# Kernel optimization log

Hardware: AMD Instinct MI355X
Metric: run time of the kernel (lower is better)

The kernel has to match this reference:

```python
import jax, jax.numpy as jnp
import numpy as np

WINDOW = 3
RATIO = 5


def _box_filter(x, win):
    """Depthwise 3D box (mean) filter, 'same' padding, per channel.
    x: [N, C, D, H, W] -> [N, C, D, H, W]
    Matches torch conv3d with ones([1,1,w,w,w])/w^3 applied per channel.
    """
    c = x.shape[1]
    k = jnp.ones((c, 1, win, win, win), x.dtype) / (win ** 3)
    pad = win // 2
    return jax.lax.conv_general_dilated(
        x, k,
        window_strides=(1, 1, 1),
        padding=[(pad, pad)] * 3,
        dimension_numbers=('NCDHW', 'OIDHW', 'NCDHW'),
        feature_group_count=c,
    )


def setup_inputs() -> dict:
    key = jax.random.key(0)
    k1, k2 = jax.random.split(key)
    y_pred = jax.random.normal(k1, (1, 3, 192, 192, 192), dtype=jnp.float32)
    y_true = jax.random.uniform(k2, (1, 1, 192, 192, 192), dtype=jnp.float32)
    return {"y_pred": y_pred, "y_true": y_true}


def reference(y_pred, y_true):
    # Finite differences (abs), each [1, 3, D-1, H-1, W-1]
    base = y_pred[:, :, :-1, :-1, :-1]
    dy = jnp.abs(y_pred[:, :, 1:, :-1, :-1] - base)
    dx = jnp.abs(y_pred[:, :, :-1, 1:, :-1] - base)
    dz = jnp.abs(y_pred[:, :, :-1, :-1, 1:] - base)

    # 9 box-filtered single-channel maps == 3 depthwise box filters
    fx = _box_filter(dx, WINDOW)
    fy = _box_filter(dy, WINDOW)
    fz = _box_filter(dz, WINDOW)
    dxdx, dxdy, dxdz = fx[:, 1:2], fy[:, 1:2], fz[:, 1:2]
    dydx, dydy, dydz = fx[:, 0:1], fy[:, 0:1], fz[:, 0:1]
    dzdx, dzdy, dzdz = fx[:, 2:3], fy[:, 2:3], fz[:, 2:3]

    # Neo-Hookean invariants
    det_1 = (dxdx + 1) * ((dydy + 1) * (dzdz + 1) - dydz * dzdy)
    det_2 = -dxdy * (dydx * (dzdz + 1) - dydz * dzdx)
    det_3 = dxdz * (dydx * dzdy - (dydy + 1) * dzdx)
    J = det_1 + det_2 + det_3

    Tr = ((dxdx + 1) ** 2 + dxdy ** 2 + dxdz ** 2
          + dydx ** 2 + (dydy + 1) ** 2 + dydz ** 2
          + dzdx ** 2 + dzdy ** 2 + (dzdz + 1) ** 2)

    # mode == 'exp'
    stretch = Tr * jnp.exp(-J + 1) - 3
    vol_change = (J - 1) ** 2

    # Faithful replication of the sequential mu/lambda normalization in torch:
    mu = 1.0
    lam = mu * RATIO
    mu = mu / (mu + lam)          # 1/6
    lam = lam / (mu + lam)        # 30/31 (uses updated mu, as in source)

    U = mu / 2 * stretch + lam / 2 * vol_change
    return jnp.mean(U)
```

## Files before the change

### kernel.cpp

```cpp
#include <hip/hip_runtime.h>
#include <math.h>

#define DIM 192
#define OD  191
#define VOLX 7077888
#define TW 32
#define TH 16
#define NBW 6
#define NBH 12
#define CD  10
#define NCH 20

typedef _Float16 h4 __attribute__((ext_vector_type(4)));
typedef _Float16 h8 __attribute__((ext_vector_type(8)));
typedef unsigned int u2v __attribute__((ext_vector_type(2)));

static __device__ __forceinline__ h4 habs4(h4 v) {
    u2v u = __builtin_bit_cast(u2v, v);
    u &= 0x7FFF7FFFu;
    return __builtin_bit_cast(h4, u);
}

__global__ __launch_bounds__(256, 4)
void nh_fused_kernel(const float* __restrict__ P, float* __restrict__ out) {
    const int tid = threadIdx.x;
    const int tx  = tid & 15;
    const int ty  = tid >> 4;
    const int w0  = blockIdx.x * TW;
    const int h0  = blockIdx.y * TH;
    const int ds  = blockIdx.z * CD;
    const int de  = min(ds + CD, OD);

    __shared__ h4 sraw[2][19][36];
    __shared__ h8 sHD[18][35];
    __shared__ h4 sW[18][38];
    __shared__ float wsum[4];

    const int oh  = h0 + ty;
    const int ow0 = w0 + 2 * tx;
    const bool v0 = (oh < OD) && (ow0 < OD);
    const bool v1 = (oh < OD) && (ow0 + 1 < OD);
    const bool interior = (w0 >= 1) && (w0 + 33 <= OD) && (h0 >= 1) && (h0 + 17 <= OD);

    h8 rA0[2], rA1[2], rA2[2];
    h4 rW0[2], rW1[2], rW2[2];
    #pragma unroll
    for (int o = 0; o < 2; ++o) {
        rA0[o] = (h8)0; rA1[o] = (h8)0; rA2[o] = (h8)0;
        rW0[o] = (h4)0; rW1[o] = (h4)0; rW2[o] = (h4)0;
    }

    float acc = 0.f;

    for (int t = ds - 1; t <= de + 1; ++t) {
        const int cb = t & 1, pb = cb ^ 1;
        __syncthreads();

        if (t >= 0 && t < DIM) {
            const size_t pl = (size_t)t * (DIM * DIM);
            if (interior) {
                #pragma unroll
                for (int it = 0; it < 3; ++it) {
                    const int l = tid + it * 256;
                    if (l < 19 * 35) {
                        const int hh = l / 35, ww = l - hh * 35;
                        const size_t base = pl + (size_t)(h0 - 1 + hh) * DIM + (size_t)(w0 - 1 + ww);
                        const float x = P[base], y = P[base + VOLX], z = P[base + 2 * VOLX];
                        sraw[cb][hh][ww] = (h4){(_Float16)x, (_Float16)y, (_Float16)z, (_Float16)0.f};
                    }
                }
            } else {
                #pragma unroll
                for (int it = 0; it < 3; ++it) {
                    const int l = tid + it * 256;
                    if (l < 19 * 35) {
                        const int hh = l / 35, ww = l - hh * 35;
                        const int hp = h0 - 1 + hh, wp = w0 - 1 + ww;
                        float x = 0.f, y = 0.f, z = 0.f;
                        if (hp >= 0 && hp < DIM && wp >= 0 && wp < DIM) {
                            const size_t base = pl + (size_t)hp * DIM + (size_t)wp;
                            x = P[base]; y = P[base + VOLX]; z = P[base + 2 * VOLX];
                        }
                        sraw[cb][hh][ww] = (h4){(_Float16)x, (_Float16)y, (_Float16)z, (_Float16)0.f};
                    }
                }
            }
        }
        __syncthreads();

        const int p = t - 1;
        const bool pp = (t >= ds) && (p >= 0) && (p < OD);
        if (pp) {
            #pragma unroll
            for (int it = 0; it < 3; ++it) {
                const int l = tid + it * 256;
                if (l < 18 * 34) {
                    const int hh = l / 34, ww = l - hh * 34;
                    const h4 c = sraw[pb][hh][ww];
                    h4 hd = habs4(sraw[pb][hh + 1][ww] - c);
                    h4 wd = habs4(sraw[pb][hh][ww + 1] - c);
                    h4 dd = habs4(sraw[cb][hh][ww] - c);
                    if (!interior) {
                        const int hp = h0 - 1 + hh, wp = w0 - 1 + ww;
                        if (hp < 0 || hp >= OD || wp < 0 || wp >= OD) {
                            hd = (h4)0; dd = (h4)0; wd = (h4)0;
                        }
                    }
                    sHD[hh][ww] = __builtin_shufflevector(hd, dd, 0, 1, 2, 3, 4, 5, 6, 7);
                    sW[hh][ww]  = wd;
                }
            }
        }
        __syncthreads();

        #pragma unroll
        for (int o = 0; o < 2; ++o) {
            rA0[o] = rA1[o]; rA1[o] = rA2[o];
            rW0[o] = rW1[o]; rW1[o] = rW2[o];
        }
        if (pp) {
            h8 s0 = (h8)0, s1 = (h8)0;
            h4 q0 = (h4)0, q1 = (h4)0;
            #pragma unroll
            for (int j = 0; j < 3; ++j) {
                const h8 t0 = sHD[ty + j][2 * tx + 0];
                const h8 t1 = sHD[ty + j][2 * tx + 1];
                const h8 t2 = sHD[ty + j][2 * tx + 2];
                const h8 t3 = sHD[ty + j][2 * tx + 3];
                const h8 m = t1 + t2;
                s0 += t0 + m;
                s1 += t3 + m;
                const h8* rw = (const h8*)&sW[ty + j][2 * tx];
                const h8 u01 = rw[0];
                const h8 u23 = rw[1];
                const h4 u0 = __builtin_shufflevector(u01, u01, 0, 1, 2, 3);
                const h4 u1 = __builtin_shufflevector(u01, u01, 4, 5, 6, 7);
                const h4 u2 = __builtin_shufflevector(u23, u23, 0, 1, 2, 3);
                const h4 u3 = __builtin_shufflevector(u23, u23, 4, 5, 6, 7);
                const h4 mw = u1 + u2;
                q0 += u0 + mw;
                q1 += u3 + mw;
            }
            rA2[0] = s0; rA2[1] = s1; rW2[0] = q0; rW2[1] = q1;
        } else {
            rA2[0] = (h8)0; rA2[1] = (h8)0; rW2[0] = (h4)0; rW2[1] = (h4)0;
        }

        const int d = t - 2;
        if (d >= ds && d < de) {
            #pragma unroll
            for (int o = 0; o < 2; ++o) {
                if (o == 0 ? v0 : v1) {
                    const h8 FA = rA0[o] + rA1[o] + rA2[o];
                    const h4 FW = rW0[o] + rW1[o] + rW2[o];
                    const float inv27 = 1.f / 27.f;
                    const float dydx = (float)FA[0] * inv27, dxdx = (float)FA[1] * inv27, dzdx = (float)FA[2] * inv27;
                    const float dydy = (float)FA[4] * inv27, dxdy = (float)FA[5] * inv27, dzdy = (float)FA[6] * inv27;
                    const float dydz = (float)FW[0] * inv27, dxdz = (float)FW[1] * inv27, dzdz = (float)FW[2] * inv27;
                    const float a = dxdx + 1.f, e = dydy + 1.f, iN = dzdz + 1.f;
                    const float J = a * (e * iN - dydz * dzdy)
                                  - dxdy * (dydx * iN - dydz * dzdx)
                                  + dxdz * (dydx * dzdy - e * dzdx);
                    const float Tr = a * a + dxdy * dxdy + dxdz * dxdz
                                   + dydx * dydx + e * e + dydz * dydz
                                   + dzdx * dzdx + dzdy * dzdy + iN * iN;
                    const float stretch = Tr * __expf(1.f - J) - 3.f;
                    const float vol = (J - 1.f) * (J - 1.f);
                    acc += 0.0833333358f * stretch + 0.4838709677f * vol;
                }
            }
        }
    }

    acc *= (1.f / 6967871.f);

    #pragma unroll
    for (int off = 32; off > 0; off >>= 1) acc += __shfl_down(acc, off, 64);
    if ((tid & 63) == 0) wsum[tid >> 6] = acc;
    __syncthreads();
    if (tid == 0) {
        atomicAdd(out, wsum[0] + wsum[1] + wsum[2] + wsum[3]);
    }
}

extern "C" void kernel_launch(void* const* d_in, const int* in_sizes, int n_in,
                              void* d_out, int out_size, void* d_ws, size_t ws_size,
                              hipStream_t stream) {
    const float* y_pred = (const float*)d_in[0];
    float* out = (float*)d_out;

    hipMemsetAsync(out, 0, sizeof(float), stream);

    dim3 grid(NBW, NBH, NCH);
    nh_fused_kernel<<<grid, 256, 0, stream>>>(y_pred, out);
}
```

Baseline: 197.6 us.

## Prefetch next plane into registers and repack difference layout into fewer LDS slots

Restructures the depth loop so each plane's global loads are issued two iterations ahead into registers and written to LDS one iteration later. This overlaps memory latency with compute and removes one barrier per plane. It precomputes clamped offsets and masks once per thread, and packs two of the three W-difference channels into the spare slots of the h8 array, leaving only one half in a small side array, which cuts LDS traffic. The depth chunk shrinks to 8 and the occupancy hint rises to 6 blocks per CU. In exchange it adds register pressure and more halo recompute from the shorter depth chunks.

Result: faster. 192.7 us (-2.5%).

```diff
diff --git a/kernel.cpp b/kernel.cpp
--- a/kernel.cpp
+++ b/kernel.cpp
@@ -3,16 +3,26 @@
 
 #define DIM 192
 #define OD  191
+#define PLN 36864
 #define VOLX 7077888
 #define TW 32
 #define TH 16
 #define NBW 6
 #define NBH 12
-#define CD  10
-#define NCH 20
-
-typedef _Float16 h4 __attribute__((ext_vector_type(4)));
-typedef _Float16 h8 __attribute__((ext_vector_type(8)));
+#define CD  8
+#define NCH 24
+
+#define RH 19
+#define RW 35
+#define NS (RH*RW)
+#define DH 18
+#define DW 34
+#define ND (DH*DW)
+#define SBW 34
+
+typedef _Float16 h2v __attribute__((ext_vector_type(2)));
+typedef _Float16 h4  __attribute__((ext_vector_type(4)));
+typedef _Float16 h8  __attribute__((ext_vector_type(8)));
 typedef unsigned int u2v __attribute__((ext_vector_type(2)));
 
 static __device__ __forceinline__ h4 habs4(h4 v) {
@@ -21,93 +31,116 @@
     return __builtin_bit_cast(h4, u);
 }
 
-__global__ __launch_bounds__(256, 4)
+__global__ __launch_bounds__(256, 6)
 void nh_fused_kernel(const float* __restrict__ P, float* __restrict__ out) {
     const int tid = threadIdx.x;
-    const int tx  = tid & 15;
-    const int ty  = tid >> 4;
-    const int w0  = blockIdx.x * TW;
-    const int h0  = blockIdx.y * TH;
-    const int ds  = blockIdx.z * CD;
-    const int de  = min(ds + CD, OD);
-
-    __shared__ h4 sraw[2][19][36];
-    __shared__ h8 sHD[18][35];
-    __shared__ h4 sW[18][38];
+    const int tx = tid & 15, ty = tid >> 4;
+    const int w0 = blockIdx.x * TW, h0 = blockIdx.y * TH;
+    const int ds = blockIdx.z * CD;
+    const int de = min(ds + CD, OD);
+    const int lastP = min(de + 1, DIM - 1);
+
+    __shared__ h4  sraw[2][RH][RW];
+    __shared__ h8  sA[DH][RW];
+    __shared__ h2v sB[DH][SBW];
     __shared__ float wsum[4];
 
-    const int oh  = h0 + ty;
-    const int ow0 = w0 + 2 * tx;
+    const int oh = h0 + ty, ow0 = w0 + 2 * tx;
     const bool v0 = (oh < OD) && (ow0 < OD);
     const bool v1 = (oh < OD) && (ow0 + 1 < OD);
-    const bool interior = (w0 >= 1) && (w0 + 33 <= OD) && (h0 >= 1) && (h0 + 17 <= OD);
+
+    int  sLin[3], sOff[3];
+    bool sMask[3], sAct[3];
+    #pragma unroll
+    for (int i = 0; i < 3; ++i) {
+        int l = tid + 256 * i;
+        sAct[i] = (l < NS);
+        l = min(l, NS - 1);
+        const int sh = l / RW, sw = l - sh * RW;
+        const int hp = h0 - 1 + sh, wp = w0 - 1 + sw;
+        sMask[i] = (hp >= 0) && (hp < DIM) && (wp >= 0) && (wp < DIM);
+        sOff[i]  = min(max(hp, 0), DIM - 1) * DIM + min(max(wp, 0), DIM - 1);
+        sLin[i]  = l;
+    }
+
+    int  dLin[3], dLinB[3];
+    bool dAct[3], dOut[3];
+    #pragma unroll
+    for (int i = 0; i < 3; ++i) {
+        int l = tid + 256 * i;
+        dAct[i] = (l < ND);
+        l = min(l, ND - 1);
+        const int dh = l / DW, dw = l - dh * DW;
+        const int hp = h0 - 1 + dh, wp = w0 - 1 + dw;
+        dOut[i]  = (hp < 0) || (hp >= OD) || (wp < 0) || (wp >= OD);
+        dLin[i]  = dh * RW + dw;
+        dLinB[i] = dh * SBW + dw;
+    }
+
+    float px[3][3];
+    #pragma unroll
+    for (int i = 0; i < 3; ++i) { px[i][0] = px[i][1] = px[i][2] = 0.f; }
+
+    auto issue = [&](int q) {
+        #pragma unroll
+        for (int i = 0; i < 3; ++i) {
+            if (sAct[i]) {
+                const float* b = P + (size_t)q * PLN + sOff[i];
+                px[i][0] = b[0]; px[i][1] = b[VOLX]; px[i][2] = b[2 * VOLX];
+            }
+        }
+    };
+    auto store = [&](int slot) {
+        h4* dst = &sraw[slot][0][0];
+        #pragma unroll
+        for (int i = 0; i < 3; ++i) {
+            if (sAct[i]) {
+                h4 v = sMask[i] ? (h4){(_Float16)px[i][0], (_Float16)px[i][1],
+                                       (_Float16)px[i][2], (_Float16)0.f}
+                                : (h4)0;
+                dst[sLin[i]] = v;
+            }
+        }
+    };
+
+    if (ds >= 1) { issue(ds - 1); store((ds - 1) & 1); }
+    issue(ds);
 
     h8 rA0[2], rA1[2], rA2[2];
-    h4 rW0[2], rW1[2], rW2[2];
+    _Float16 rB0[2], rB1[2], rB2[2];
     #pragma unroll
     for (int o = 0; o < 2; ++o) {
         rA0[o] = (h8)0; rA1[o] = (h8)0; rA2[o] = (h8)0;
-        rW0[o] = (h4)0; rW1[o] = (h4)0; rW2[o] = (h4)0;
-    }
-
+        rB0[o] = (_Float16)0.f; rB1[o] = (_Float16)0.f; rB2[o] = (_Float16)0.f;
+    }
     float acc = 0.f;
 
-    for (int t = ds - 1; t <= de + 1; ++t) {
-        const int cb = t & 1, pb = cb ^ 1;
+    for (int p = ds - 1; p <= de; ++p) {
+        const int sp = p & 1, sn = sp ^ 1;
+        const bool pv = (p >= 0) && (p < OD);
+
+        if (p + 1 <= lastP) store(sn);
+        if (p + 2 <= lastP) issue(p + 2);
         __syncthreads();
 
-        if (t >= 0 && t < DIM) {
-            const size_t pl = (size_t)t * (DIM * DIM);
-            if (interior) {
-                #pragma unroll
-                for (int it = 0; it < 3; ++it) {
-                    const int l = tid + it * 256;
-                    if (l < 19 * 35) {
-                        const int hh = l / 35, ww = l - hh * 35;
-                        const size_t base = pl + (size_t)(h0 - 1 + hh) * DIM + (size_t)(w0 - 1 + ww);
-                        const float x = P[base], y = P[base + VOLX], z = P[base + 2 * VOLX];
-                        sraw[cb][hh][ww] = (h4){(_Float16)x, (_Float16)y, (_Float16)z, (_Float16)0.f};
-                    }
-                }
-            } else {
-                #pragma unroll
-                for (int it = 0; it < 3; ++it) {
-                    const int l = tid + it * 256;
-                    if (l < 19 * 35) {
-                        const int hh = l / 35, ww = l - hh * 35;
-                        const int hp = h0 - 1 + hh, wp = w0 - 1 + ww;
-                        float x = 0.f, y = 0.f, z = 0.f;
-                        if (hp >= 0 && hp < DIM && wp >= 0 && wp < DIM) {
-                            const size_t base = pl + (size_t)hp * DIM + (size_t)wp;
-                            x = P[base]; y = P[base + VOLX]; z = P[base + 2 * VOLX];
-                        }
-                        sraw[cb][hh][ww] = (h4){(_Float16)x, (_Float16)y, (_Float16)z, (_Float16)0.f};
-                    }
-                }
-            }
-        }
-        __syncthreads();
-
-        const int p = t - 1;
-        const bool pp = (t >= ds) && (p >= 0) && (p < OD);
-        if (pp) {
+        if (pv) {
+            const h4* rp = &sraw[sp][0][0];
+            const h4* rn = &sraw[sn][0][0];
+            h8*  pA = &sA[0][0];
+            h2v* pB = &sB[0][0];
             #pragma unroll
-            for (int it = 0; it < 3; ++it) {
-                const int l = tid + it * 256;
-                if (l < 18 * 34) {
-                    const int hh = l / 34, ww = l - hh * 34;
-                    const h4 c = sraw[pb][hh][ww];
-                    h4 hd = habs4(sraw[pb][hh + 1][ww] - c);
-                    h4 wd = habs4(sraw[pb][hh][ww + 1] - c);
-                    h4 dd = habs4(sraw[cb][hh][ww] - c);
-                    if (!interior) {
-                        const int hp = h0 - 1 + hh, wp = w0 - 1 + ww;
-                        if (hp < 0 || hp >= OD || wp < 0 || wp >= OD) {
-                            hd = (h4)0; dd = (h4)0; wd = (h4)0;
-                        }
-                    }
-                    sHD[hh][ww] = __builtin_shufflevector(hd, dd, 0, 1, 2, 3, 4, 5, 6, 7);
-                    sW[hh][ww]  = wd;
+            for (int i = 0; i < 3; ++i) {
+                if (dAct[i]) {
+                    const int li = dLin[i];
+                    const h4 c  = rp[li];
+                    h4 hd = habs4(rp[li + RW] - c);
+                    h4 wd = habs4(rp[li + 1]  - c);
+                    h4 dd = habs4(rn[li]      - c);
+                    if (dOut[i]) { hd = (h4)0; wd = (h4)0; dd = (h4)0; }
+                    const h4 lo = __builtin_shufflevector(hd, wd, 0, 1, 2, 4);
+                    const h4 hi = __builtin_shufflevector(dd, wd, 0, 1, 2, 5);
+                    pA[li] = __builtin_shufflevector(lo, hi, 0, 1, 2, 3, 4, 5, 6, 7);
+                    pB[dLinB[i]] = (h2v){wd[2], (_Float16)0.f};
                 }
             }
         }
@@ -116,47 +149,43 @@
         #pragma unroll
         for (int o = 0; o < 2; ++o) {
             rA0[o] = rA1[o]; rA1[o] = rA2[o];
-            rW0[o] = rW1[o]; rW1[o] = rW2[o];
-        }
-        if (pp) {
+            rB0[o] = rB1[o]; rB1[o] = rB2[o];
+        }
+        if (pv) {
             h8 s0 = (h8)0, s1 = (h8)0;
-            h4 q0 = (h4)0, q1 = (h4)0;
+            _Float16 q0 = (_Float16)0.f, q1 = (_Float16)0.f;
             #pragma unroll
             for (int j = 0; j < 3; ++j) {
-                const h8 t0 = sHD[ty + j][2 * tx + 0];
-                const h8 t1 = sHD[ty + j][2 * tx + 1];
-                const h8 t2 = sHD[ty + j][2 * tx + 2];
-                const h8 t3 = sHD[ty + j][2 * tx + 3];
+                const h8* rowA = &sA[ty + j][2 * tx];
+                const h8 t0 = rowA[0], t1 = rowA[1], t2 = rowA[2], t3 = rowA[3];
+                const h4* rowB = (const h4*)&sB[ty + j][2 * tx];
+                const h4 u01 = rowB[0], u23 = rowB[1];
                 const h8 m = t1 + t2;
                 s0 += t0 + m;
                 s1 += t3 + m;
-                const h8* rw = (const h8*)&sW[ty + j][2 * tx];
-                const h8 u01 = rw[0];
-                const h8 u23 = rw[1];
-                const h4 u0 = __builtin_shufflevector(u01, u01, 0, 1, 2, 3);
-                const h4 u1 = __builtin_shufflevector(u01, u01, 4, 5, 6, 7);
-                const h4 u2 = __builtin_shufflevector(u23, u23, 0, 1, 2, 3);
-                const h4 u3 = __builtin_shufflevector(u23, u23, 4, 5, 6, 7);
-                const h4 mw = u1 + u2;
-                q0 += u0 + mw;
-                q1 += u3 + mw;
-            }
-            rA2[0] = s0; rA2[1] = s1; rW2[0] = q0; rW2[1] = q1;
+                const _Float16 mB = u01[2] + u23[0];
+                q0 += u01[0] + mB;
+                q1 += u23[2] + mB;
+            }
+            rA2[0] = s0; rA2[1] = s1; rB2[0] = q0; rB2[1] = q1;
         } else {
-            rA2[0] = (h8)0; rA2[1] = (h8)0; rW2[0] = (h4)0; rW2[1] = (h4)0;
-        }
-
-        const int d = t - 2;
-        if (d >= ds && d < de) {
+            rA2[0] = (h8)0; rA2[1] = (h8)0;
+            rB2[0] = (_Float16)0.f; rB2[1] = (_Float16)0.f;
+        }
+
+        const int d = p - 1;
+        if (d >= ds) {
             #pragma unroll
             for (int o = 0; o < 2; ++o) {
                 if (o == 0 ? v0 : v1) {
                     const h8 FA = rA0[o] + rA1[o] + rA2[o];
-                    const h4 FW = rW0[o] + rW1[o] + rW2[o];
+                    const float FBz = (float)(rB0[o] + rB1[o] + rB2[o]);
                     const float inv27 = 1.f / 27.f;
                     const float dydx = (float)FA[0] * inv27, dxdx = (float)FA[1] * inv27, dzdx = (float)FA[2] * inv27;
+                    const float dydz = (float)FA[3] * inv27;
                     const float dydy = (float)FA[4] * inv27, dxdy = (float)FA[5] * inv27, dzdy = (float)FA[6] * inv27;
-                    const float dydz = (float)FW[0] * inv27, dxdz = (float)FW[1] * inv27, dzdz = (float)FW[2] * inv27;
+                    const float dxdz = (float)FA[7] * inv27;
+                    const float dzdz = FBz * inv27;
                     const float a = dxdx + 1.f, e = dydy + 1.f, iN = dzdz + 1.f;
                     const float J = a * (e * iN - dydz * dzdy)
                                   - dxdy * (dydx * iN - dydz * dzdx)
```
